# Kernel optimization log

Hardware: AMD Instinct MI355X
Metric: run time of the kernel (lower is better)

Reference implementation:

```python
import jax, jax.numpy as jnp
import numpy as np

EPS = 1e-06

def setup_inputs() -> dict:
    key = jax.random.key(0)
    k1, k2, k3, k4 = jax.random.split(key, 4)
    B, N, H, W = 8, 8, 512, 512
    pd_rgbo = jax.random.normal(k1, (B, 4, H, W), dtype=jnp.float32)
    gt_rgbo = jax.random.normal(k2, (B, 4, H, W), dtype=jnp.float32)
    pd_mask = jax.random.randint(k3, (B, N, H, W), 0, 2, dtype=jnp.int32)
    gt_mask = jax.random.randint(k4, (B, N, H, W), 0, 2, dtype=jnp.int32)
    return {"pd_rgbo": pd_rgbo, "gt_rgbo": gt_rgbo, "pd_mask": pd_mask, "gt_mask": gt_mask}

def reference(pd_rgbo, gt_rgbo, pd_mask, gt_mask):
    # masks -> bool, derived mask combinations
    pm = pd_mask.astype(bool)            # [B,N,H,W]
    gm = gt_mask.astype(bool)
    dt = pd_rgbo.dtype
    pmf = pm.astype(dt)
    and_f = (pm & gm).astype(dt)         # logical_and
    xor_f = (pm & ~gm).astype(dt)        # xor(or, gt) == pd & ~gt
    gmf = gm.astype(dt)

    pd_rgb = pd_rgbo[:, :3]              # [B,3,H,W]
    gt_rgb = gt_rgbo[:, :3]
    pd_o = jnp.round(pd_rgbo[:, 3])      # [B,H,W]
    gt_o = jnp.round(gt_rgbo[:, 3])

    # per-pixel L2 color distance over channels: [B,H,W]
    diff_norm = jnp.linalg.norm(pd_rgb - gt_rgb, ord=2, axis=1)

    # punish: mean color distance over predicted-mask pixels (per b,n)
    sim_sum = jnp.einsum('bhw,bnhw->bn', diff_norm, pmf)
    count = jnp.sum(pmf, axis=(2, 3))
    punish = sim_sum / (count + EPS)

    # IoU from rounded opacities masked by logical masks
    inter = jnp.einsum('bhw,bnhw->bn', pd_o, and_f)
    gt_sum = jnp.einsum('bhw,bnhw->bn', gt_o, gmf)
    pd_xor_sum = jnp.einsum('bhw,bnhw->bn', pd_o, xor_f)
    iou = inter / (gt_sum + pd_xor_sum + EPS)

    # weights default to ones -> plain mean over all (b, n) pairs
    loss = jnp.mean(1.0 - iou + punish)
    return loss
```

## Files before the change

kernel.cpp:

```cpp
#include <hip/hip_runtime.h>


constexpr int Bc  = 8;
constexpr int Nc  = 8;
constexpr int HWc = 512 * 512;
constexpr int BPI = 1024;
constexpr float EPSc = 1e-6f;

__device__ __forceinline__ float wave_reduce(float v) {
#pragma unroll
    for (int off = 32; off; off >>= 1) v += __shfl_xor(v, off, 64);
    return v;
}

template<bool USE_PART>
__global__ __launch_bounds__(256) void niou_partial(
    const float* __restrict__ pd, const float* __restrict__ gt,
    const int* __restrict__ pmask, const int* __restrict__ gmask,
    float* __restrict__ outp )
{
    __shared__ float dnL[264], poL[264], goL[264];

    const int tid  = threadIdx.x;
    const int b    = blockIdx.x >> 10;
    const int blk  = blockIdx.x & 1023;
    const int base = blk * 256;
    const int pix  = base + tid;

    const float* pdB = pd + (size_t)b * 4 * HWc + pix;
    const float* gtB = gt + (size_t)b * 4 * HWc + pix;
    float pr[4], gr[4];
#pragma unroll
    for (int c = 0; c < 4; ++c) pr[c] = pdB[(size_t)c * HWc];
#pragma unroll
    for (int c = 0; c < 4; ++c) gr[c] = gtB[(size_t)c * HWc];

    const int g = tid >> 6, q = tid & 63;
    const int qb = base + 4 * q;
    int4 pmv[2], gmv[2];
    pmv[0] = *reinterpret_cast<const int4*>(pmask + (size_t)(b * Nc + 2 * g    ) * HWc + qb);
    gmv[0] = *reinterpret_cast<const int4*>(gmask + (size_t)(b * Nc + 2 * g    ) * HWc + qb);
    pmv[1] = *reinterpret_cast<const int4*>(pmask + (size_t)(b * Nc + 2 * g + 1) * HWc + qb);
    gmv[1] = *reinterpret_cast<const int4*>(gmask + (size_t)(b * Nc + 2 * g + 1) * HWc + qb);
    __builtin_amdgcn_sched_barrier(0);

    {
        const float dx = pr[0] - gr[0], dy = pr[1] - gr[1], dz = pr[2] - gr[2];
        const int si = tid + (tid >> 5);
        dnL[si] = sqrtf(dx * dx + dy * dy + dz * dz);
        poL[si] = rintf(pr[3]);
        goL[si] = rintf(gr[3]);
    }
    __syncthreads();

    float dn[4], po[4], go[4];
#pragma unroll
    for (int j = 0; j < 4; ++j) {
        const int p4 = 4 * q + j, s4 = p4 + (p4 >> 5);
        dn[j] = dnL[s4]; po[j] = poL[s4]; go[j] = goL[s4];
    }

    float acc[2][4];
    int   wcnt[2];
#pragma unroll
    for (int pp = 0; pp < 2; ++pp) {
        wcnt[pp] = 0;
#pragma unroll
        for (int k = 0; k < 4; ++k) acc[pp][k] = 0.f;
    }

#pragma unroll
    for (int pp = 0; pp < 2; ++pp) {
        const int pmx[4] = {pmv[pp].x, pmv[pp].y, pmv[pp].z, pmv[pp].w};
        const int gmx[4] = {gmv[pp].x, gmv[pp].y, gmv[pp].z, gmv[pp].w};
#pragma unroll
        for (int j = 0; j < 4; ++j) {
            const bool P = pmx[j] != 0;
            const bool G = gmx[j] != 0;
            wcnt[pp] += __popcll(__ballot(P));
            const float s = P ? po[j] : 0.f;
            acc[pp][0] += P ? dn[j] : 0.f;
            acc[pp][1] += G ? s     : 0.f;
            acc[pp][2] += G ? go[j] : 0.f;
            acc[pp][3] += s;
        }
    }

    const int lane = tid & 63;
#pragma unroll
    for (int pp = 0; pp < 2; ++pp) {
        const float s0 = wave_reduce(acc[pp][0]);
        const float s1 = wave_reduce(acc[pp][1]);
        const float s2 = wave_reduce(acc[pp][2]);
        const float s3 = wave_reduce(acc[pp][3]);
        if (lane == 0) {
            const int n = 2 * g + pp;
            if (USE_PART) {
                float* dst = outp + (size_t)(b * 40 + n * 5) * BPI + blk;
                dst[0 * BPI] = s0;
                dst[1 * BPI] = (float)wcnt[pp];
                dst[2 * BPI] = s1;
                dst[3 * BPI] = s2;
                dst[4 * BPI] = s3;
            } else {
                float* wsn = outp + (size_t)(b * 40 + n * 5) * 16;
                atomicAdd(&wsn[0 * 16], s0);
                atomicAdd(&wsn[1 * 16], (float)wcnt[pp]);
                atomicAdd(&wsn[2 * 16], s1);
                atomicAdd(&wsn[3 * 16], s2);
                atomicAdd(&wsn[4 * 16], s3);
            }
        }
    }
}

__global__ __launch_bounds__(256) void niou_reduce(
    const float* __restrict__ part, float* __restrict__ sums)
{
    const int slot = blockIdx.x;
    const int tid  = threadIdx.x;
    float s = 0.f;
#pragma unroll
    for (int i = 0; i < BPI; i += 256) s += part[(size_t)slot * BPI + i + tid];
    s = wave_reduce(s);
    __shared__ float w4[4];
    if ((tid & 63) == 0) w4[tid >> 6] = s;
    __syncthreads();
    if (tid == 0) sums[slot] = w4[0] + w4[1] + w4[2] + w4[3];
}

__global__ __launch_bounds__(64) void niou_final(
    const float* __restrict__ w0, float* __restrict__ out, int pad)
{
    const int t = threadIdx.x;
    const float* w = w0 + (size_t)t * 5 * pad;
    const float sim   = w[0 * pad];
    const float cnt   = w[1 * pad];
    const float inter = w[2 * pad];
    const float gts   = w[3 * pad];
    const float ssum  = w[4 * pad];
    const float xo    = ssum - inter;
    const float punish = sim / (cnt + EPSc);
    const float iou    = inter / (gts + xo + EPSc);
    float term = 1.0f - iou + punish;
#pragma unroll
    for (int off = 32; off; off >>= 1) term += __shfl_xor(term, off, 64);
    if (t == 0) out[0] = term * (1.0f / 64.0f);
}

extern "C" void kernel_launch(void* const* d_in, const int* in_sizes, int n_in,
                              void* d_out, int out_size, void* d_ws, size_t ws_size,
                              hipStream_t stream) {
    const float* pd_rgbo = (const float*)d_in[0];
    const float* gt_rgbo = (const float*)d_in[1];
    const int*   pd_mask = (const int*)d_in[2];
    const int*   gt_mask = (const int*)d_in[3];
    float* out = (float*)d_out;
    float* ws  = (float*)d_ws;

    const size_t need = ((size_t)320 * BPI + 320) * sizeof(float);
    if (ws_size >= need) {
        float* part = ws;
        float* sums = ws + (size_t)320 * BPI;
        niou_partial<true><<<Bc * BPI, 256, 0, stream>>>(pd_rgbo, gt_rgbo,
                                                         pd_mask, gt_mask, part);
        niou_reduce<<<320, 256, 0, stream>>>(part, sums);
        niou_final<<<1, 64, 0, stream>>>(sums, out, 1);
    } else {
        hipMemsetAsync(ws, 0, 320 * 16 * sizeof(float), stream);
        niou_partial<false><<<Bc * BPI, 256, 0, stream>>>(pd_rgbo, gt_rgbo,
                                                          pd_mask, gt_mask, ws);
        niou_final<<<1, 64, 0, stream>>>(ws, out, 16);
    }
}
```

Before: 40.98 us.

## Double pixels per block with inline-asm loads and staged vmcnt waits

Each block now handles 512 pixels instead of 256: every thread loads float2 colour data and two int4 mask vectors per mask plane, and the grid shrinks to 512 blocks per batch. Loads use inline-asm global_load instructions with explicit s_waitcnt so the colour math and LDS staging can start while the mask loads are still in flight. LDS padding is dropped in favour of vectorised float2/float4 accesses, and the partials buffer and reduce kernel shrink to match. The trade is more registers per thread (occupancy hint of 4) and reliance on hand-counted vmcnt values being correct.

Result: faster. 38.61 us (-5.8%).

```diff
diff --git a/kernel.cpp b/kernel.cpp
--- a/kernel.cpp
+++ b/kernel.cpp
@@ -4,8 +4,23 @@
 constexpr int Bc  = 8;
 constexpr int Nc  = 8;
 constexpr int HWc = 512 * 512;
-constexpr int BPI = 1024;
+constexpr int BPI = 512;
 constexpr float EPSc = 1e-6f;
+
+__device__ __forceinline__ float2 gload_f2(const float* a) {
+    float2 r;
+    asm volatile("global_load_dwordx2 %0, %1, off" : "=v"(r) : "v"(a) : "memory");
+    return r;
+}
+__device__ __forceinline__ int4 gload_i4(const int* a) {
+    int4 r;
+    asm volatile("global_load_dwordx4 %0, %1, off" : "=v"(r) : "v"(a) : "memory");
+    return r;
+}
+#define WAITV(n_) do {                                                   \
+        asm volatile("s_waitcnt vmcnt(" #n_ ")" ::: "memory");           \
+        __builtin_amdgcn_sched_barrier(0);                               \
+    } while (0)
 
 __device__ __forceinline__ float wave_reduce(float v) {
 #pragma unroll
@@ -14,50 +29,61 @@
 }
 
 template<bool USE_PART>
-__global__ __launch_bounds__(256) void niou_partial(
+__global__ __launch_bounds__(256, 4) void niou_partial(
     const float* __restrict__ pd, const float* __restrict__ gt,
     const int* __restrict__ pmask, const int* __restrict__ gmask,
     float* __restrict__ outp )
 {
-    __shared__ float dnL[264], poL[264], goL[264];
+    __shared__ float dnL[512], poL[512], goL[512];
 
     const int tid  = threadIdx.x;
-    const int b    = blockIdx.x >> 10;
-    const int blk  = blockIdx.x & 1023;
-    const int base = blk * 256;
-    const int pix  = base + tid;
-
-    const float* pdB = pd + (size_t)b * 4 * HWc + pix;
-    const float* gtB = gt + (size_t)b * 4 * HWc + pix;
-    float pr[4], gr[4];
-#pragma unroll
-    for (int c = 0; c < 4; ++c) pr[c] = pdB[(size_t)c * HWc];
-#pragma unroll
-    for (int c = 0; c < 4; ++c) gr[c] = gtB[(size_t)c * HWc];
+    const int b    = blockIdx.x >> 9;
+    const int blk  = blockIdx.x & 511;
+    const int base = blk * 512;
+
+    const float* pdB = pd + (size_t)b * 4 * HWc + base + 2 * tid;
+    const float* gtB = gt + (size_t)b * 4 * HWc + base + 2 * tid;
+    float2 pr[4], gr[4];
+#pragma unroll
+    for (int c = 0; c < 4; ++c) pr[c] = gload_f2(pdB + (size_t)c * HWc);
+#pragma unroll
+    for (int c = 0; c < 4; ++c) gr[c] = gload_f2(gtB + (size_t)c * HWc);
 
     const int g = tid >> 6, q = tid & 63;
-    const int qb = base + 4 * q;
-    int4 pmv[2], gmv[2];
-    pmv[0] = *reinterpret_cast<const int4*>(pmask + (size_t)(b * Nc + 2 * g    ) * HWc + qb);
-    gmv[0] = *reinterpret_cast<const int4*>(gmask + (size_t)(b * Nc + 2 * g    ) * HWc + qb);
-    pmv[1] = *reinterpret_cast<const int4*>(pmask + (size_t)(b * Nc + 2 * g + 1) * HWc + qb);
-    gmv[1] = *reinterpret_cast<const int4*>(gmask + (size_t)(b * Nc + 2 * g + 1) * HWc + qb);
-    __builtin_amdgcn_sched_barrier(0);
-
+    int4 pmv[2][2], gmv[2][2];
+#pragma unroll
+    for (int pp = 0; pp < 2; ++pp) {
+        const size_t pl = (size_t)(b * Nc + 2 * g + pp) * HWc + base + 4 * q;
+#pragma unroll
+        for (int qq = 0; qq < 2; ++qq) {
+            pmv[pp][qq] = gload_i4(pmask + pl + 256 * qq);
+            gmv[pp][qq] = gload_i4(gmask + pl + 256 * qq);
+        }
+    }
+
+    WAITV(8);
     {
-        const float dx = pr[0] - gr[0], dy = pr[1] - gr[1], dz = pr[2] - gr[2];
-        const int si = tid + (tid >> 5);
-        dnL[si] = sqrtf(dx * dx + dy * dy + dz * dz);
-        poL[si] = rintf(pr[3]);
-        goL[si] = rintf(gr[3]);
+        const float dx0 = pr[0].x - gr[0].x, dy0 = pr[1].x - gr[1].x, dz0 = pr[2].x - gr[2].x;
+        const float dx1 = pr[0].y - gr[0].y, dy1 = pr[1].y - gr[1].y, dz1 = pr[2].y - gr[2].y;
+        float2 d2, p2, g2;
+        d2.x = sqrtf(dx0*dx0 + dy0*dy0 + dz0*dz0);
+        d2.y = sqrtf(dx1*dx1 + dy1*dy1 + dz1*dz1);
+        p2.x = rintf(pr[3].x); p2.y = rintf(pr[3].y);
+        g2.x = rintf(gr[3].x); g2.y = rintf(gr[3].y);
+        *reinterpret_cast<float2*>(&dnL[2 * tid]) = d2;
+        *reinterpret_cast<float2*>(&poL[2 * tid]) = p2;
+        *reinterpret_cast<float2*>(&goL[2 * tid]) = g2;
     }
     __syncthreads();
 
-    float dn[4], po[4], go[4];
-#pragma unroll
-    for (int j = 0; j < 4; ++j) {
-        const int p4 = 4 * q + j, s4 = p4 + (p4 >> 5);
-        dn[j] = dnL[s4]; po[j] = poL[s4]; go[j] = goL[s4];
+    WAITV(0);
+    float4 dnq[2], poq[2], goq[2];
+#pragma unroll
+    for (int qq = 0; qq < 2; ++qq) {
+        const int li = 256 * qq + 4 * q;
+        dnq[qq] = *reinterpret_cast<const float4*>(&dnL[li]);
+        poq[qq] = *reinterpret_cast<const float4*>(&poL[li]);
+        goq[qq] = *reinterpret_cast<const float4*>(&goL[li]);
     }
 
     float acc[2][4];
@@ -70,21 +96,26 @@
     }
 
 #pragma unroll
-    for (int pp = 0; pp < 2; ++pp) {
-        const int pmx[4] = {pmv[pp].x, pmv[pp].y, pmv[pp].z, pmv[pp].w};
-        const int gmx[4] = {gmv[pp].x, gmv[pp].y, gmv[pp].z, gmv[pp].w};
-#pragma unroll
-        for (int j = 0; j < 4; ++j) {
-            const bool P = pmx[j] != 0;
-            const bool G = gmx[j] != 0;
-            wcnt[pp] += __popcll(__ballot(P));
-            const float s = P ? po[j] : 0.f;
-            acc[pp][0] += P ? dn[j] : 0.f;
-            acc[pp][1] += G ? s     : 0.f;
-            acc[pp][2] += G ? go[j] : 0.f;
-            acc[pp][3] += s;
+    for (int pp = 0; pp < 2; ++pp)
+#pragma unroll
+        for (int qq = 0; qq < 2; ++qq) {
+            const int pmx[4] = {pmv[pp][qq].x, pmv[pp][qq].y, pmv[pp][qq].z, pmv[pp][qq].w};
+            const int gmx[4] = {gmv[pp][qq].x, gmv[pp][qq].y, gmv[pp][qq].z, gmv[pp][qq].w};
+            const float dnj[4] = {dnq[qq].x, dnq[qq].y, dnq[qq].z, dnq[qq].w};
+            const float poj[4] = {poq[qq].x, poq[qq].y, poq[qq].z, poq[qq].w};
+            const float goj[4] = {goq[qq].x, goq[qq].y, goq[qq].z, goq[qq].w};
+#pragma unroll
+            for (int j = 0; j < 4; ++j) {
+                const bool P = pmx[j] != 0;
+                const bool G = gmx[j] != 0;
+                wcnt[pp] += __popcll(__ballot(P));
+                const float s = P ? poj[j] : 0.f;
+                acc[pp][0] += P ? dnj[j] : 0.f;
+                acc[pp][1] += G ? s      : 0.f;
+                acc[pp][2] += G ? goj[j] : 0.f;
+                acc[pp][3] += s;
+            }
         }
-    }
 
     const int lane = tid & 63;
 #pragma unroll
```
